# Kernel optimization log

Measured on AMD Instinct MI355X. Metric: run time of the kernel, lower is better.

## Reference

```python
import jax, jax.numpy as jnp
import numpy as np

D_MODEL = 1024
N_HEADS = 16
HEAD_DIM = D_MODEL // N_HEADS
B, T = 4, 2048


def setup_inputs() -> dict:
    key = jax.random.key(0)
    ks = jax.random.split(key, 9)
    s = 1.0 / np.sqrt(D_MODEL)
    x = jax.random.normal(ks[0], (B, T, D_MODEL), dtype=jnp.float32)
    # causal mask: 1 = attend, 0 = blocked (masked_fill(mask == 0, -inf))
    mask = jnp.tril(jnp.ones((T, T), dtype=jnp.int32))[None, None, :, :]
    Wq = jax.random.uniform(ks[1], (D_MODEL, D_MODEL), jnp.float32, -s, s)
    bq = jax.random.uniform(ks[2], (D_MODEL,), jnp.float32, -s, s)
    Wk = jax.random.uniform(ks[3], (D_MODEL, D_MODEL), jnp.float32, -s, s)
    bk = jax.random.uniform(ks[4], (D_MODEL,), jnp.float32, -s, s)
    Wv = jax.random.uniform(ks[5], (D_MODEL, D_MODEL), jnp.float32, -s, s)
    bv = jax.random.uniform(ks[6], (D_MODEL,), jnp.float32, -s, s)
    Wo = jax.random.uniform(ks[7], (D_MODEL, D_MODEL), jnp.float32, -s, s)
    bo = jax.random.uniform(ks[8], (D_MODEL,), jnp.float32, -s, s)
    return {"x": x, "mask": mask, "Wq": Wq, "bq": bq, "Wk": Wk, "bk": bk,
            "Wv": Wv, "bv": bv, "Wo": Wo, "bo": bo}


def reference(x, mask, Wq, bq, Wk, bk, Wv, bv, Wo, bo):
    # nn.Linear: y = x @ W.T + b; here W stored as [in, out] so y = x @ W + b
    Bsz, Tlen, C = x.shape
    scale = jnp.sqrt(jnp.float32(HEAD_DIM))

    def split_heads(t):  # [B,T,C] -> [B,H,T,hd]
        return t.reshape(Bsz, Tlen, N_HEADS, HEAD_DIM).transpose(0, 2, 1, 3)

    Q = split_heads(x @ Wq + bq)
    K = split_heads(x @ Wk + bk)
    V = split_heads(x @ Wv + bv)

    scores = jnp.einsum("bhqd,bhkd->bhqk", Q, K) / scale
    scores = jnp.where(mask == 0, jnp.float32(-jnp.inf), scores)
    weights = jax.nn.softmax(scores, axis=-1)  # dropout is identity (eval/p=0)
    out = jnp.einsum("bhqk,bhkd->bhqd", weights, V)
    out = out.transpose(0, 2, 1, 3).reshape(Bsz, Tlen, C)
    return out @ Wo + bo
```

## Files before the change

### kernel.cpp

```cpp
#include <hip/hip_runtime.h>
#include <cstdint>
#include <cstddef>

#define B_SZ 4
#define T_SZ 2048
#define NH 16
#define HD 64
#define CD 1024
#define MROWS (B_SZ*T_SZ)
#define NEG_BIG (-1e30f)
#define Q_SCALE 0.180336880f

typedef __bf16 bf16x8 __attribute__((ext_vector_type(8)));
typedef __bf16 bf16x4 __attribute__((ext_vector_type(4)));
typedef short s16x4 __attribute__((ext_vector_type(4)));
typedef float f32x4 __attribute__((ext_vector_type(4)));

typedef __attribute__((address_space(3))) void* as3p;
typedef const __attribute__((address_space(1))) void* as1p;

__device__ __forceinline__ void glds16(const void* g, void* l) {
  __builtin_amdgcn_global_load_lds((as1p)g, (as3p)l, 16, 0, 0);
}

__global__ __launch_bounds__(256) void detect_dtype(const uint32_t* __restrict__ x,
                                                    int* __restrict__ flag) {
  __shared__ int cnt[256];
  const int t = threadIdx.x;
  int c = 0;
  for (int i = 0; i < 4; i++) {
    uint32_t w = x[t * 4 + i];
    uint32_t e = (w >> 7) & 0xFF;
    c += (e >= 100 && e <= 140) ? 1 : 0;
  }
  cnt[t] = c;
  __syncthreads();
  for (int s = 128; s > 0; s >>= 1) {
    if (t < s) cnt[t] += cnt[t + s];
    __syncthreads();
  }
  if (t == 0) flag[0] = (cnt[0] > 700) ? 1 : 0;
}

__device__ __forceinline__ bf16x8 cvt8(const void* src, int isbf, size_t i8) {
  bf16x8 o;
  if (isbf) {
    o = ((const bf16x8*)src)[i8];
  } else {
    const float4* s = (const float4*)((const float*)src + i8 * 8);
    float4 a = s[0], b = s[1];
    o[0] = (__bf16)a.x; o[1] = (__bf16)a.y; o[2] = (__bf16)a.z; o[3] = (__bf16)a.w;
    o[4] = (__bf16)b.x; o[5] = (__bf16)b.y; o[6] = (__bf16)b.z; o[7] = (__bf16)b.w;
  }
  return o;
}

__global__ __launch_bounds__(256) void conv_in(const void* __restrict__ src,
                                               const int* __restrict__ flag,
                                               __bf16* __restrict__ dst, int n8) {
  int i = blockIdx.x * 256 + threadIdx.x;
  if (i >= n8) return;
  ((bf16x8*)dst)[i] = cvt8(src, flag[0], i);
}

struct Ptr4 { const void* s[4]; __bf16* d[4]; };

__global__ __launch_bounds__(256) void conv_b4(Ptr4 p, const int* __restrict__ flag) {
  int i = threadIdx.x;
  if (i >= CD / 8) return;
  int which = blockIdx.x;
  ((bf16x8*)p.d[which])[i] = cvt8(p.s[which], flag[0], i);
}

__global__ __launch_bounds__(256) void transpose_conv4(Ptr4 p,
                                                       const int* __restrict__ flag) {
  __shared__ __align__(16) __bf16 tile[64 * 72];
  const void* W = p.s[blockIdx.z];
  __bf16* WT = p.d[blockIdx.z];
  const int t = threadIdx.x;
  const int r0 = blockIdx.y * 64, c0 = blockIdx.x * 64;
  const int rr = t >> 3, c8 = (t & 7) * 8;
  const int isbf = flag[0];
  for (int pp = 0; pp < 2; pp++) {
    int r = pp * 32 + rr;
    *(bf16x8*)(tile + r * 72 + c8) =
        cvt8(W, isbf, ((size_t)(r0 + r) * CD + c0 + c8) / 8);
  }
  __syncthreads();
  for (int pp = 0; pp < 2; pp++) {
    int cc = pp * 32 + rr;
    bf16x8 o;
    for (int j = 0; j < 8; j++) o[j] = tile[(c8 + j) * 72 + cc];
    *(bf16x8*)(WT + (size_t)(c0 + cc) * CD + r0 + c8) = o;
  }
}

__global__ __launch_bounds__(256) void gemm_qkv(
    const __bf16* __restrict__ A, const __bf16* __restrict__ BT,
    const __bf16* __restrict__ bias,
    __bf16* __restrict__ Qb, __bf16* __restrict__ Kb, __bf16* __restrict__ Vt) {
  __shared__ __align__(16) __bf16 As[128 * 64];
  __shared__ __align__(16) __bf16 Bs[128 * 64];
  const int tid = threadIdx.x;
  const int w = tid >> 6, lane = tid & 63;
  const int l15 = lane & 15, quad = lane >> 4;
  const int wm = w & 1, wn = w >> 1;
  const int bm = blockIdx.y, bn = blockIdx.x;

  f32x4 acc[4][4];
  for (int i = 0; i < 4; i++)
    for (int j = 0; j < 4; j++) acc[i][j] = (f32x4)0.f;

  const int srow = lane >> 3, scol = (lane & 7) * 8;
  const __bf16* Abase = A + (size_t)(bm * 128) * CD;
  const __bf16* Bbase = BT + (size_t)(bn * 128) * CD;

  for (int k0 = 0; k0 < CD; k0 += 64) {
    __syncthreads();
    for (int p = 0; p < 4; p++) {
      int seg = p * 4 + w;
      int row = seg * 8 + srow;
      glds16(Abase + (size_t)row * CD + k0 + scol, (char*)As + seg * 1024);
      glds16(Bbase + (size_t)row * CD + k0 + scol, (char*)Bs + seg * 1024);
    }
    __syncthreads();
    for (int kc = 0; kc < 2; kc++) {
      const int koff = kc * 32 + quad * 8;
      bf16x8 af[4], bfr[4];
      for (int mt = 0; mt < 4; mt++)
        af[mt] = *(const bf16x8*)(As + (wm * 64 + mt * 16 + l15) * 64 + koff);
      for (int nt = 0; nt < 4; nt++)
        bfr[nt] = *(const bf16x8*)(Bs + (wn * 64 + nt * 16 + l15) * 64 + koff);
      for (int mt = 0; mt < 4; mt++)
        for (int nt = 0; nt < 4; nt++)
          acc[mt][nt] = __builtin_amdgcn_mfma_f32_16x16x32_bf16(
              af[mt], bfr[nt], acc[mt][nt], 0, 0, 0);
    }
  }

  for (int nt = 0; nt < 4; nt++) {
    int col = bn * 128 + wn * 64 + nt * 16 + l15;
    int seg = col >> 10;
    int c = col & 1023, h = c >> 6, d = c & 63;
    float bv = (float)bias[col];
    for (int mt = 0; mt < 4; mt++) {
      int row0 = bm * 128 + wm * 64 + mt * 16 + quad * 4;
      int b = row0 >> 11, tok0 = row0 & 2047;
      if (seg == 2) {
        bf16x4 o;
        for (int r = 0; r < 4; r++) o[r] = (__bf16)(acc[mt][nt][r] + bv);
        *(bf16x4*)(Vt + ((size_t)((b << 4) + h) * HD + d) * T_SZ + tok0) = o;
      } else {
        __bf16* dst = (seg == 0) ? Qb : Kb;
        float sc = (seg == 0) ? Q_SCALE : 1.f;
        for (int r = 0; r < 4; r++) {
          float v = (acc[mt][nt][r] + bv) * sc;
          dst[((size_t)(b * NH + h) * T_SZ + tok0 + r) * HD + d] = (__bf16)v;
        }
      }
    }
  }
}

__global__ __launch_bounds__(256) void gemm_out(
    const __bf16* __restrict__ A, const __bf16* __restrict__ BT,
    const __bf16* __restrict__ bias, void* __restrict__ Out,
    const int* __restrict__ flag) {
  __shared__ __align__(16) __bf16 As[128 * 64];
  __shared__ __align__(16) __bf16 Bs[128 * 64];
  const int tid = threadIdx.x;
  const int w = tid >> 6, lane = tid & 63;
  const int l15 = lane & 15, quad = lane >> 4;
  const int wm = w & 1, wn = w >> 1;
  const int bm = blockIdx.y, bn = blockIdx.x;

  f32x4 acc[4][4];
  for (int i = 0; i < 4; i++)
    for (int j = 0; j < 4; j++) acc[i][j] = (f32x4)0.f;

  const int srow = lane >> 3, scol = (lane & 7) * 8;
  const __bf16* Abase = A + (size_t)(bm * 128) * CD;
  const __bf16* Bbase = BT + (size_t)(bn * 128) * CD;

  for (int k0 = 0; k0 < CD; k0 += 64) {
    __syncthreads();
    for (int p = 0; p < 4; p++) {
      int seg = p * 4 + w;
      int row = seg * 8 + srow;
      glds16(Abase + (size_t)row * CD + k0 + scol, (char*)As + seg * 1024);
      glds16(Bbase + (size_t)row * CD + k0 + scol, (char*)Bs + seg * 1024);
    }
    __syncthreads();
    for (int kc = 0; kc < 2; kc++) {
      const int koff = kc * 32 + quad * 8;
      bf16x8 af[4], bfr[4];
      for (int mt = 0; mt < 4; mt++)
        af[mt] = *(const bf16x8*)(As + (wm * 64 + mt * 16 + l15) * 64 + koff);
      for (int nt = 0; nt < 4; nt++)
        bfr[nt] = *(const bf16x8*)(Bs + (wn * 64 + nt * 16 + l15) * 64 + koff);
      for (int mt = 0; mt < 4; mt++)
        for (int nt = 0; nt < 4; nt++)
          acc[mt][nt] = __builtin_amdgcn_mfma_f32_16x16x32_bf16(
              af[mt], bfr[nt], acc[mt][nt], 0, 0, 0);
    }
  }

  const int isbf = flag[0];
  for (int nt = 0; nt < 4; nt++) {
    int col = bn * 128 + wn * 64 + nt * 16 + l15;
    float bv = (float)bias[col];
    for (int mt = 0; mt < 4; mt++) {
      int row0 = bm * 128 + wm * 64 + mt * 16 + quad * 4;
      if (isbf) {
        for (int r = 0; r < 4; r++)
          ((__bf16*)Out)[(size_t)(row0 + r) * CD + col] =
              (__bf16)(acc[mt][nt][r] + bv);
      } else {
        for (int r = 0; r < 4; r++)
          ((float*)Out)[(size_t)(row0 + r) * CD + col] = acc[mt][nt][r] + bv;
      }
    }
  }
}

__global__ __launch_bounds__(512) void attn(
    const __bf16* __restrict__ Q, const __bf16* __restrict__ K,
    const __bf16* __restrict__ Vt, __bf16* __restrict__ Y) {
  __shared__ __align__(16) __bf16 Ks[2][64 * 72];
  __shared__ __align__(16) __bf16 Vs[2][64 * 72];

  const int tid = threadIdx.x, w = tid >> 6, lane = tid & 63;
  const int l15 = lane & 15, quad = lane >> 4;
  const int bh = blockIdx.y;
  const int pairi = blockIdx.x;

  const __bf16* Qbh = Q + (size_t)bh * T_SZ * HD;
  const __bf16* Kbh = K + (size_t)bh * T_SZ * HD;
  const __bf16* Vbh = Vt + (size_t)bh * HD * T_SZ;

  const int srow = tid >> 3;
  const int scol = (tid & 7) * 8;
  const int b = bh >> 4, h = bh & 15;

  for (int ph = 0; ph < 2; ph++) {
    const int tq = ph ? (7 - pairi) : pairi;
    const int q0 = tq * 256;
    const int niter = 4 * tq + 4;

    __syncthreads();
    *(bf16x8*)(Ks[0] + srow * 72 + scol) =
        *(const bf16x8*)(Kbh + (size_t)srow * HD + scol);
    *(bf16x8*)(Vs[0] + srow * 72 + scol) =
        *(const bf16x8*)(Vbh + (size_t)srow * T_SZ + scol);

    bf16x8 aq[2][2];
    for (int mt = 0; mt < 2; mt++)
      for (int kc = 0; kc < 2; kc++)
        aq[mt][kc] = *(const bf16x8*)(
            Qbh + (size_t)(q0 + w * 32 + mt * 16 + l15) * HD + kc * 32 + quad * 8);

    f32x4 acco[2][4];
    for (int mt = 0; mt < 2; mt++)
      for (int dt = 0; dt < 4; dt++) acco[mt][dt] = (f32x4)0.f;
    float m_[2], l_[2];
    for (int mt = 0; mt < 2; mt++) { m_[mt] = NEG_BIG; l_[mt] = 0.f; }

    for (int it = 0; it < niter; it++) {
      const int cur = it & 1;
      const int kv0 = it * 64;
      __syncthreads();

      bf16x8 kn, vn;
      const bool havenext = (it + 1 < niter);
      if (havenext) {
        int kv1 = kv0 + 64;
        kn = *(const bf16x8*)(Kbh + (size_t)(kv1 + srow) * HD + scol);
        vn = *(const bf16x8*)(Vbh + (size_t)srow * T_SZ + kv1 + scol);
      }

      const __bf16* Ksc = Ks[cur];
      const __bf16* Vsc = Vs[cur];

      f32x4 accs[2][4];
      for (int mt = 0; mt < 2; mt++)
        for (int nt = 0; nt < 4; nt++) accs[mt][nt] = (f32x4)0.f;
      for (int kc = 0; kc < 2; kc++)
        for (int nt = 0; nt < 4; nt++) {
          bf16x8 ak = *(const bf16x8*)(Ksc + (nt * 16 + l15) * 72 + kc * 32 + quad * 8);
          for (int mt = 0; mt < 2; mt++)
            accs[mt][nt] = __builtin_amdgcn_mfma_f32_16x16x32_bf16(
                ak, aq[mt][kc], accs[mt][nt], 0, 0, 0);
        }

      for (int mt = 0; mt < 2; mt++) {
        if (kv0 + 63 > q0 + w * 32 + mt * 16) {
          int qg = q0 + w * 32 + mt * 16 + l15;
          for (int nt = 0; nt < 4; nt++) {
            int kg0 = kv0 + nt * 16 + quad * 4;
            for (int r = 0; r < 4; r++)
              if (kg0 + r > qg) accs[mt][nt][r] = NEG_BIG;
          }
        }
      }

      float mloc[2], alpha[2], rs[2];
      for (int mt = 0; mt < 2; mt++) {
        float a0 = fmaxf(fmaxf(accs[mt][0][0], accs[mt][0][1]),
                         fmaxf(accs[mt][0][2], accs[mt][0][3]));
        float a1 = fmaxf(fmaxf(accs[mt][1][0], accs[mt][1][1]),
                         fmaxf(accs[mt][1][2], accs[mt][1][3]));
        float a2 = fmaxf(fmaxf(accs[mt][2][0], accs[mt][2][1]),
                         fmaxf(accs[mt][2][2], accs[mt][2][3]));
        float a3 = fmaxf(fmaxf(accs[mt][3][0], accs[mt][3][1]),
                         fmaxf(accs[mt][3][2], accs[mt][3][3]));
        mloc[mt] = fmaxf(fmaxf(a0, a1), fmaxf(a2, a3));
      }
      for (int off = 16; off < 64; off <<= 1)
        for (int mt = 0; mt < 2; mt++)
          mloc[mt] = fmaxf(mloc[mt], __shfl_xor(mloc[mt], off));
      for (int mt = 0; mt < 2; mt++) {
        float mnew = fmaxf(m_[mt], mloc[mt]);
        alpha[mt] = exp2f(m_[mt] - mnew);
        m_[mt] = mnew;
        rs[mt] = 0.f;
      }

      bf16x4 pf[2][4];
      for (int mt = 0; mt < 2; mt++)
        for (int nt = 0; nt < 4; nt++)
          for (int r = 0; r < 4; r++) {
            float p = exp2f(accs[mt][nt][r] - m_[mt]);
            rs[mt] += p;
            pf[mt][nt][r] = (__bf16)p;
          }
      for (int off = 16; off < 64; off <<= 1)
        for (int mt = 0; mt < 2; mt++) rs[mt] += __shfl_xor(rs[mt], off);
      for (int mt = 0; mt < 2; mt++) l_[mt] = l_[mt] * alpha[mt] + rs[mt];
      for (int mt = 0; mt < 2; mt++)
        for (int dt = 0; dt < 4; dt++)
          for (int r = 0; r < 4; r++) acco[mt][dt][r] *= alpha[mt];

      for (int nt = 0; nt < 4; nt++)
        for (int dt = 0; dt < 4; dt++) {
          bf16x4 av = *(const bf16x4*)(Vsc + (dt * 16 + l15) * 72 + nt * 16 + quad * 4);
          for (int mt = 0; mt < 2; mt++)
            acco[mt][dt] = __builtin_amdgcn_mfma_f32_16x16x16bf16_1k(
                *(const s16x4*)&av, *(const s16x4*)&pf[mt][nt], acco[mt][dt], 0, 0, 0);
        }

      if (havenext) {
        int nb = cur ^ 1;
        *(bf16x8*)(Ks[nb] + srow * 72 + scol) = kn;
        *(bf16x8*)(Vs[nb] + srow * 72 + scol) = vn;
      }
    }

    for (int mt = 0; mt < 2; mt++) {
      float rcp = 1.f / l_[mt];
      int qg = q0 + w * 32 + mt * 16 + l15;
      size_t base = ((size_t)(b * T_SZ + qg)) * CD + h * HD + quad * 4;
      for (int dt = 0; dt < 4; dt++) {
        bf16x4 o;
        for (int r = 0; r < 4; r++) o[r] = (__bf16)(acco[mt][dt][r] * rcp);
        *(bf16x4*)(Y + base + dt * 16) = o;
      }
    }
  }
}

extern "C" void kernel_launch(void* const* d_in, const int* in_sizes, int n_in,
                              void* d_out, int out_size, void* d_ws, size_t ws_size,
                              hipStream_t stream) {
  (void)in_sizes; (void)n_in; (void)out_size; (void)ws_size;
  const void* x  = d_in[0];
  const void* Wq = d_in[2];
  const void* bq = d_in[3];
  const void* Wk = d_in[4];
  const void* bk = d_in[5];
  const void* Wv = d_in[6];
  const void* bv = d_in[7];
  const void* Wo = d_in[8];
  const void* bo = d_in[9];

  char* ws = (char*)d_ws;
  const size_t MB = 1024 * 1024;
  __bf16* WqkvT = (__bf16*)(ws + 0 * MB);
  __bf16* WoT   = (__bf16*)(ws + 6 * MB);
  __bf16* bqkvc = (__bf16*)(ws + 8 * MB);
  __bf16* boc   = (__bf16*)(ws + 8 * MB + 8192);
  int*    flag  = (int*)   (ws + 8 * MB + 65536);
  __bf16* xc    = (__bf16*)(ws + 9 * MB);
  __bf16* Qb    = (__bf16*)(ws + 25 * MB);
  __bf16* Kb    = (__bf16*)(ws + 41 * MB);
  __bf16* Vt_g  = (__bf16*)(ws + 57 * MB);
  __bf16* Yb    = xc;

  dim3 tb(256);
  detect_dtype<<<1, tb, 0, stream>>>((const uint32_t*)x, flag);

  conv_in<<<4096, tb, 0, stream>>>(x, flag, xc, MROWS * CD / 8);
  Ptr4 pb = {{bq, bk, bv, bo}, {bqkvc, bqkvc + CD, bqkvc + 2 * CD, boc}};
  conv_b4<<<4, tb, 0, stream>>>(pb, flag);
  Ptr4 pw = {{Wq, Wk, Wv, Wo},
             {WqkvT, WqkvT + (size_t)CD * CD, WqkvT + 2 * (size_t)CD * CD, WoT}};
  transpose_conv4<<<dim3(16, 16, 4), tb, 0, stream>>>(pw, flag);

  gemm_qkv<<<dim3(24, MROWS / 128), tb, 0, stream>>>(xc, WqkvT, bqkvc, Qb, Kb, Vt_g);

  attn<<<dim3(4, B_SZ * NH), dim3(512), 0, stream>>>(Qb, Kb, Vt_g, Yb);

  gemm_out<<<dim3(CD / 128, MROWS / 128), tb, 0, stream>>>(Yb, WoT, boc, d_out, flag);
}
```

Before: 326.6 us.

## Halve attention query tile, double grid, skip masked tiles and lazy rescale

The attention kernel now gives each block 128 queries instead of 256, with one 16-row tile per warp, and launches twice as many blocks with a remapped block index that groups heads together. Warps skip KV tiles that lie fully above the causal diagonal. The online-softmax rescale runs only when the running max increases, and the V shared-memory stride is padded to 76 to cut bank conflicts. The aim is more parallelism, better load balance and less wasted causal work, at the cost of less K/V reuse per block, more barrier overhead per unit of work, and warp divergence near the diagonal.

```diff
diff --git a/kernel.cpp b/kernel.cpp
--- a/kernel.cpp
+++ b/kernel.cpp
@@ -223,16 +223,17 @@
   }
 }
 
-__global__ __launch_bounds__(512) void attn(
+__global__ __launch_bounds__(512, 4) void attn(
     const __bf16* __restrict__ Q, const __bf16* __restrict__ K,
     const __bf16* __restrict__ Vt, __bf16* __restrict__ Y) {
   __shared__ __align__(16) __bf16 Ks[2][64 * 72];
-  __shared__ __align__(16) __bf16 Vs[2][64 * 72];
+  __shared__ __align__(16) __bf16 Vs[2][64 * 76];
 
   const int tid = threadIdx.x, w = tid >> 6, lane = tid & 63;
   const int l15 = lane & 15, quad = lane >> 4;
-  const int bh = blockIdx.y;
-  const int pairi = blockIdx.x;
+  const int lid = blockIdx.x + 8 * blockIdx.y;
+  const int bh = lid & 63;
+  const int pairi = lid >> 6;
 
   const __bf16* Qbh = Q + (size_t)bh * T_SZ * HD;
   const __bf16* Kbh = K + (size_t)bh * T_SZ * HD;
@@ -243,27 +244,28 @@
   const int b = bh >> 4, h = bh & 15;
 
   for (int ph = 0; ph < 2; ph++) {
-    const int tq = ph ? (7 - pairi) : pairi;
-    const int q0 = tq * 256;
-    const int niter = 4 * tq + 4;
+    const int tq = ph ? (15 - pairi) : pairi;
+    const int q0 = tq * 128;
+    const int niter = 2 * tq + 2;
+    const int qw = q0 + w * 16;
 
     __syncthreads();
     *(bf16x8*)(Ks[0] + srow * 72 + scol) =
         *(const bf16x8*)(Kbh + (size_t)srow * HD + scol);
-    *(bf16x8*)(Vs[0] + srow * 72 + scol) =
-        *(const bf16x8*)(Vbh + (size_t)srow * T_SZ + scol);
-
-    bf16x8 aq[2][2];
-    for (int mt = 0; mt < 2; mt++)
-      for (int kc = 0; kc < 2; kc++)
-        aq[mt][kc] = *(const bf16x8*)(
-            Qbh + (size_t)(q0 + w * 32 + mt * 16 + l15) * HD + kc * 32 + quad * 8);
-
-    f32x4 acco[2][4];
-    for (int mt = 0; mt < 2; mt++)
-      for (int dt = 0; dt < 4; dt++) acco[mt][dt] = (f32x4)0.f;
-    float m_[2], l_[2];
-    for (int mt = 0; mt < 2; mt++) { m_[mt] = NEG_BIG; l_[mt] = 0.f; }
+    {
+      bf16x8 v0 = *(const bf16x8*)(Vbh + (size_t)srow * T_SZ + scol);
+      *(bf16x4*)(Vs[0] + srow * 76 + scol)     = ((bf16x4*)&v0)[0];
+      *(bf16x4*)(Vs[0] + srow * 76 + scol + 4) = ((bf16x4*)&v0)[1];
+    }
+
+    bf16x8 aq[2];
+    for (int kc = 0; kc < 2; kc++)
+      aq[kc] = *(const bf16x8*)(
+          Qbh + (size_t)(qw + l15) * HD + kc * 32 + quad * 8);
+
+    f32x4 acco[4];
+    for (int dt = 0; dt < 4; dt++) acco[dt] = (f32x4)0.f;
+    float m_ = NEG_BIG, l_ = 0.f;
 
     for (int it = 0; it < niter; it++) {
       const int cur = it & 1;
@@ -278,90 +280,84 @@
         vn = *(const bf16x8*)(Vbh + (size_t)srow * T_SZ + kv1 + scol);
       }
 
-      const __bf16* Ksc = Ks[cur];
-      const __bf16* Vsc = Vs[cur];
-
-      f32x4 accs[2][4];
-      for (int mt = 0; mt < 2; mt++)
-        for (int nt = 0; nt < 4; nt++) accs[mt][nt] = (f32x4)0.f;
-      for (int kc = 0; kc < 2; kc++)
-        for (int nt = 0; nt < 4; nt++) {
-          bf16x8 ak = *(const bf16x8*)(Ksc + (nt * 16 + l15) * 72 + kc * 32 + quad * 8);
-          for (int mt = 0; mt < 2; mt++)
-            accs[mt][nt] = __builtin_amdgcn_mfma_f32_16x16x32_bf16(
-                ak, aq[mt][kc], accs[mt][nt], 0, 0, 0);
-        }
-
-      for (int mt = 0; mt < 2; mt++) {
-        if (kv0 + 63 > q0 + w * 32 + mt * 16) {
-          int qg = q0 + w * 32 + mt * 16 + l15;
+      if (kv0 <= qw + 15) {
+        const __bf16* Ksc = Ks[cur];
+        const __bf16* Vsc = Vs[cur];
+
+        f32x4 accs[4];
+        for (int nt = 0; nt < 4; nt++) accs[nt] = (f32x4)0.f;
+        for (int kc = 0; kc < 2; kc++)
+          for (int nt = 0; nt < 4; nt++) {
+            bf16x8 ak = *(const bf16x8*)(Ksc + (nt * 16 + l15) * 72 + kc * 32 + quad * 8);
+            accs[nt] = __builtin_amdgcn_mfma_f32_16x16x32_bf16(
+                ak, aq[kc], accs[nt], 0, 0, 0);
+          }
+
+        if (kv0 + 63 > qw) {
+          int qg = qw + l15;
           for (int nt = 0; nt < 4; nt++) {
             int kg0 = kv0 + nt * 16 + quad * 4;
             for (int r = 0; r < 4; r++)
-              if (kg0 + r > qg) accs[mt][nt][r] = NEG_BIG;
+              if (kg0 + r > qg) accs[nt][r] = NEG_BIG;
           }
         }
-      }
-
-      float mloc[2], alpha[2], rs[2];
-      for (int mt = 0; mt < 2; mt++) {
-        float a0 = fmaxf(fmaxf(accs[mt][0][0], accs[mt][0][1]),
-                         fmaxf(accs[mt][0][2], accs[mt][0][3]));
-        float a1 = fmaxf(fmaxf(accs[mt][1][0], accs[mt][1][1]),
-                         fmaxf(accs[mt][1][2], accs[mt][1][3]));
-        float a2 = fmaxf(fmaxf(accs[mt][2][0], accs[mt][2][1]),
-                         fmaxf(accs[mt][2][2], accs[mt][2][3]));
-        float a3 = fmaxf(fmaxf(accs[mt][3][0], accs[mt][3][1]),
-                         fmaxf(accs[mt][3][2], accs[mt][3][3]));
-        mloc[mt] = fmaxf(fmaxf(a0, a1), fmaxf(a2, a3));
-      }
-      for (int off = 16; off < 64; off <<= 1)
-        for (int mt = 0; mt < 2; mt++)
-          mloc[mt] = fmaxf(mloc[mt], __shfl_xor(mloc[mt], off));
-      for (int mt = 0; mt < 2; mt++) {
-        float mnew = fmaxf(m_[mt], mloc[mt]);
-        alpha[mt] = exp2f(m_[mt] - mnew);
-        m_[mt] = mnew;
-        rs[mt] = 0.f;
-      }
-
-      bf16x4 pf[2][4];
-      for (int mt = 0; mt < 2; mt++)
+
+        float a0 = fmaxf(fmaxf(accs[0][0], accs[0][1]),
+                         fmaxf(accs[0][2], accs[0][3]));
+        float a1 = fmaxf(fmaxf(accs[1][0], accs[1][1]),
+                         fmaxf(accs[1][2], accs[1][3]));
+        float a2 = fmaxf(fmaxf(accs[2][0], accs[2][1]),
+                         fmaxf(accs[2][2], accs[2][3]));
+        float a3 = fmaxf(fmaxf(accs[3][0], accs[3][1]),
+                         fmaxf(accs[3][2], accs[3][3]));
+        float mloc = fmaxf(fmaxf(a0, a1), fmaxf(a2, a3));
+        mloc = fmaxf(mloc, __shfl_xor(mloc, 16));
+        mloc = fmaxf(mloc, __shfl_xor(mloc, 32));
+
+        if (!__all(mloc <= m_)) {
+          float mnew = fmaxf(m_, mloc);
+          float alpha = exp2f(m_ - mnew);
+          m_ = mnew;
+          l_ *= alpha;
+          for (int dt = 0; dt < 4; dt++)
+            for (int r = 0; r < 4; r++) acco[dt][r] *= alpha;
+        }
+
+        float rs = 0.f;
+        bf16x4 pf[4];
         for (int nt = 0; nt < 4; nt++)
           for (int r = 0; r < 4; r++) {
-            float p = exp2f(accs[mt][nt][r] - m_[mt]);
-            rs[mt] += p;
-            pf[mt][nt][r] = (__bf16)p;
+            float p = exp2f(accs[nt][r] - m_);
+            rs += p;
+            pf[nt][r] = (__bf16)p;
           }
-      for (int off = 16; off < 64; off <<= 1)
-        for (int mt = 0; mt < 2; mt++) rs[mt] += __shfl_xor(rs[mt], off);
-      for (int mt = 0; mt < 2; mt++) l_[mt] = l_[mt] * alpha[mt] + rs[mt];
-      for (int mt = 0; mt < 2; mt++)
-        for (int dt = 0; dt < 4; dt++)
-          for (int r = 0; r < 4; r++) acco[mt][dt][r] *= alpha[mt];
-
-      for (int nt = 0; nt < 4; nt++)
-        for (int dt = 0; dt < 4; dt++) {
-          bf16x4 av = *(const bf16x4*)(Vsc + (dt * 16 + l15) * 72 + nt * 16 + quad * 4);
-          for (int mt = 0; mt < 2; mt++)
-            acco[mt][dt] = __builtin_amdgcn_mfma_f32_16x16x16bf16_1k(
-                *(const s16x4*)&av, *(const s16x4*)&pf[mt][nt], acco[mt][dt], 0, 0, 0);
-        }
+        rs += __shfl_xor(rs, 16);
+        rs += __shfl_xor(rs, 32);
+        l_ += rs;
+
+        for (int nt = 0; nt < 4; nt++)
+          for (int dt = 0; dt < 4; dt++) {
+            bf16x4 av = *(const bf16x4*)(Vsc + (dt * 16 + l15) * 76 + nt * 16 + quad * 4);
+            acco[dt] = __builtin_amdgcn_mfma_f32_16x16x16bf16_1k(
+                *(const s16x4*)&av, *(const s16x4*)&pf[nt], acco[dt], 0, 0, 0);
+          }
+      }
 
       if (havenext) {
         int nb = cur ^ 1;
         *(bf16x8*)(Ks[nb] + srow * 72 + scol) = kn;
-        *(bf16x8*)(Vs[nb] + srow * 72 + scol) = vn;
-      }
-    }
-
-    for (int mt = 0; mt < 2; mt++) {
-      float rcp = 1.f / l_[mt];
-      int qg = q0 + w * 32 + mt * 16 + l15;
+        *(bf16x4*)(Vs[nb] + srow * 76 + scol)     = ((bf16x4*)&vn)[0];
+        *(bf16x4*)(Vs[nb] + srow * 76 + scol + 4) = ((bf16x4*)&vn)[1];
+      }
+    }
+
+    {
+      float rcp = 1.f / l_;
+      int qg = qw + l15;
       size_t base = ((size_t)(b * T_SZ + qg)) * CD + h * HD + quad * 4;
       for (int dt = 0; dt < 4; dt++) {
         bf16x4 o;
-        for (int r = 0; r < 4; r++) o[r] = (__bf16)(acco[mt][dt][r] * rcp);
+        for (int r = 0; r < 4; r++) o[r] = (__bf16)(acco[dt][r] * rcp);
         *(bf16x4*)(Y + base + dt * 16) = o;
       }
     }
@@ -407,7 +403,7 @@
 
   gemm_qkv<<<dim3(24, MROWS / 128), tb, 0, stream>>>(xc, WqkvT, bqkvc, Qb, Kb, Vt_g);
 
-  attn<<<dim3(4, B_SZ * NH), dim3(512), 0, stream>>>(Qb, Kb, Vt_g, Yb);
+  attn<<<dim3(8, B_SZ * NH), dim3(512), 0, stream>>>(Qb, Kb, Vt_g, Yb);
 
   gemm_out<<<dim3(CD / 128, MROWS / 128), tb, 0, stream>>>(Yb, WoT, boc, d_out, flag);
 }
```

Result: faster. 314.5 us (-3.7%).
